# Optimization experiments

Measured on AMD Instinct MI355X. Metric: run time of the kernel, lower is better.

## Reference

```python
import jax, jax.numpy as jnp
import numpy as np


def setup_inputs() -> dict:
    key = jax.random.key(0)
    # [B, T, H, C] feature map; cummax is taken along T (axis=1)
    inputs = jax.random.normal(key, (16, 512, 64, 128), dtype=jnp.float32)
    return {"inputs": inputs}


def reference(inputs):
    # tf.scan(maximum) over the transposed time axis == cumulative max along axis 1.
    # jax.lax.cummax lowers to a parallel associative scan (log-depth), which is the
    # efficient expression of the same math.
    return jax.lax.cummax(inputs, axis=1)
```

## Files before the change

kernel.cpp:

```cpp
#include <hip/hip_runtime.h>
#include <hip/hip_bf16.h>
#include <math.h>


#define T_DIM 512
#define HC 8192
#define B_DIM 16

__global__ __launch_bounds__(128) void cummax_kernel(const float* __restrict__ in,
                                                     float* __restrict__ out) {
    int gid = blockIdx.x * blockDim.x + threadIdx.x;
    int b   = gid >> 12;
    int cp  = gid & 4095;

    const float2* __restrict__ src =
        (const float2*)(in  + (size_t)b * T_DIM * HC) + cp;
    float2* __restrict__ dst =
        (float2*)(out + (size_t)b * T_DIM * HC) + cp;

    float mx = -INFINITY;
    float my = -INFINITY;

    #pragma unroll 8
    for (int t = 0; t < T_DIM; ++t) {
        float2 v = src[t * (HC / 2)];
        mx = fmaxf(mx, v.x);
        my = fmaxf(my, v.y);
        float2 o;
        o.x = mx;
        o.y = my;
        dst[t * (HC / 2)] = o;
    }
}

extern "C" void kernel_launch(void* const* d_in, const int* in_sizes, int n_in,
                              void* d_out, int out_size, void* d_ws, size_t ws_size,
                              hipStream_t stream) {
    const float* in = (const float*)d_in[0];
    float* out = (float*)d_out;

    dim3 grid(512);
    dim3 block(128);
    cummax_kernel<<<grid, block, 0, stream>>>(in, out);
}
```

Baseline: 418.8 us.

## Split time axis into segments with shared-memory carry for cummax

Replaces the one-thread-per-column sequential scan with a two-level segmented scan. Each block takes 32 float2 columns, splits T into 16 segments of 32 steps, and gives each segment to its own thread, which loads its 32 values into registers. Segment maxima are exchanged through shared memory to form each segment's prefix. This raises the thread count from 65536 to about a million to expose far more memory parallelism, at the cost of a 64-float register array per thread and a block barrier.

```diff
diff --git a/kernel.cpp b/kernel.cpp
--- a/kernel.cpp
+++ b/kernel.cpp
@@ -1,35 +1,64 @@
 #include <hip/hip_runtime.h>
-#include <hip/hip_bf16.h>
 #include <math.h>
 
 
 #define T_DIM 512
-#define HC 8192
+#define HC    8192
+#define HC2   4096
 #define B_DIM 16
+#define SEG   16
+#define TSEG  32
+#define COLS  32
+#define NCOL2 65536
 
-__global__ __launch_bounds__(128) void cummax_kernel(const float* __restrict__ in,
+__global__ __launch_bounds__(512, 4) void cummax_seg(const float* __restrict__ in,
                                                      float* __restrict__ out) {
-    int gid = blockIdx.x * blockDim.x + threadIdx.x;
-    int b   = gid >> 12;
-    int cp  = gid & 4095;
+    __shared__ float2 segmax[SEG][COLS];
+
+    const int tid = threadIdx.x;
+    const int c   = tid & (COLS - 1);
+    const int s   = tid >> 5;
+
+    const int col = blockIdx.x * COLS + c;
+    const int b   = col >> 12;
+    const int cp  = col & (HC2 - 1);
 
     const float2* __restrict__ src =
-        (const float2*)(in  + (size_t)b * T_DIM * HC) + cp;
+        (const float2*)(in + (size_t)b * T_DIM * HC) + (size_t)(s * TSEG) * HC2 + cp;
     float2* __restrict__ dst =
-        (float2*)(out + (size_t)b * T_DIM * HC) + cp;
+        (float2*)(out + (size_t)b * T_DIM * HC) + (size_t)(s * TSEG) * HC2 + cp;
 
-    float mx = -INFINITY;
-    float my = -INFINITY;
+    float2 v[TSEG];
+    #pragma unroll
+    for (int i = 0; i < TSEG; ++i) {
+        v[i] = src[(size_t)i * HC2];
+    }
 
-    #pragma unroll 8
-    for (int t = 0; t < T_DIM; ++t) {
-        float2 v = src[t * (HC / 2)];
-        mx = fmaxf(mx, v.x);
-        my = fmaxf(my, v.y);
+    float mx = -INFINITY, my = -INFINITY;
+    #pragma unroll
+    for (int i = 0; i < TSEG; ++i) {
+        mx = fmaxf(mx, v[i].x);
+        my = fmaxf(my, v[i].y);
+        v[i].x = mx;
+        v[i].y = my;
+    }
+
+    segmax[s][c] = make_float2(mx, my);
+    __syncthreads();
+
+    float px = -INFINITY, py = -INFINITY;
+    for (int j = 0; j < s; ++j) {
+        float2 sm = segmax[j][c];
+        px = fmaxf(px, sm.x);
+        py = fmaxf(py, sm.y);
+    }
+
+    #pragma unroll
+    for (int i = 0; i < TSEG; ++i) {
         float2 o;
-        o.x = mx;
-        o.y = my;
-        dst[t * (HC / 2)] = o;
+        o.x = fmaxf(px, v[i].x);
+        o.y = fmaxf(py, v[i].y);
+        dst[(size_t)i * HC2] = o;
     }
 }
 
@@ -39,7 +68,7 @@
     const float* in = (const float*)d_in[0];
     float* out = (float*)d_out;
 
-    dim3 grid(512);
-    dim3 block(128);
-    cummax_kernel<<<grid, block, 0, stream>>>(in, out);
+    dim3 grid(NCOL2 / COLS);
+    dim3 block(COLS * SEG);
+    cummax_seg<<<grid, block, 0, stream>>>(in, out);
 }
```

New measurement: 431.9 us. 3.1% more time.
